# Performance work log

Hardware: AMD Instinct MI355X
Metric: run time of the kernel (lower is better)

## Reference

```python
import jax, jax.numpy as jnp
import numpy as np

N_VOLS, N_PARTS = 4, 8          # hard-coded in GL.forward
B = N_VOLS * N_PARTS            # asserted batch size = 32
DIM, HID, PROJ = 8192, 4096, 256
TEMP = 0.1
BN_EPS = 1e-5


def setup_inputs() -> dict:
    key = jax.random.key(0)
    k = jax.random.split(key, 5)
    s1 = 1.0 / np.sqrt(DIM)
    s2 = 1.0 / np.sqrt(HID)
    return {
        "x": jax.random.normal(k[0], (B, DIM), jnp.float32),
        "W1": jax.random.uniform(k[1], (DIM, HID), jnp.float32, -s1, s1),
        "b1": jax.random.uniform(k[2], (HID,), jnp.float32, -s1, s1),
        "gamma": jnp.ones((HID,), jnp.float32),
        "beta": jnp.zeros((HID,), jnp.float32),
        "W2": jax.random.uniform(k[3], (HID, PROJ), jnp.float32, -s2, s2),
        "b2": jax.random.uniform(k[4], (PROJ,), jnp.float32, -s2, s2),
    }


def _gl_loss(proj):
    # F.normalize(p=2, dim=-1); CosineSimilarity on unit vectors == dot product
    p = proj / jnp.linalg.norm(proj, axis=-1, keepdims=True)
    sims = (p @ p.T) / TEMP                       # [B, B]
    idx = jnp.arange(B)
    # pos_index(i) = {i % n_parts + v * n_parts} -> same part id; includes i itself
    pos_mask = (idx[:, None] % N_PARTS) == (idx[None, :] % N_PARTS)  # [B, B], 4 per row
    neg_mask = ~pos_mask                                             # 28 per row
    E = jnp.exp(sims)                              # original uses raw exp (no max-shift)
    row_neg = jnp.sum(jnp.where(neg_mask, E, 0.0), axis=1)    # sum_j exp(s[i, neg_j])
    ET = E.T                                        # ET[i, p] = exp(s[p, i])
    col_neg = jnp.sum(jnp.where(neg_mask, ET, 0.0), axis=1)   # sum_j exp(s[neg_j, i])
    t1 = -jnp.log(E / (E + row_neg[:, None]))      # row-direction term per (i, pos)
    t2 = -jnp.log(ET / (ET + col_neg[:, None]))    # column-direction term per (i, pos)
    per_row = jnp.sum(jnp.where(pos_mask, t1 + t2, 0.0), axis=1) / N_VOLS
    return jnp.sum(per_row) / (B * 2)


def reference(x, W1, b1, gamma, beta, W2, b2):
    # projector MLP: Linear -> BatchNorm1d (training stats) -> ReLU -> Linear
    h = x @ W1 + b1
    mu = jnp.mean(h, axis=0)
    var = jnp.var(h, axis=0)                       # biased variance, BN training mode
    h = gamma * (h - mu) * jax.lax.rsqrt(var + BN_EPS) + beta
    h = jax.nn.relu(h)
    proj = h @ W2 + b2                             # [B, PROJ]
    return _gl_loss(proj)
```

## Files before the change

### kernel.cpp

```cpp
#include <hip/hip_runtime.h>

#define DIM   8192
#define HID   4096
#define PROJ  256
#define NB    32
#define KSP1  16
#define KCH1  (DIM / KSP1)
#define KT1   (KCH1 / 32)
#define KSP2  16
#define KCH2  (HID / KSP2)
#define KT2   (KCH2 / 32)

typedef __attribute__((ext_vector_type(8))) short bf16x8;
typedef __attribute__((ext_vector_type(4))) float f32x4;

__device__ __forceinline__ float bf2f(unsigned short u) {
    return __uint_as_float(((unsigned)u) << 16);
}
__device__ __forceinline__ unsigned short f2bf(float f) {
    unsigned u = __float_as_uint(f);
    u += 0x7fffu + ((u >> 16) & 1u);
    return (unsigned short)(u >> 16);
}
__device__ __forceinline__ unsigned pk2(float a, float b) {
    return (unsigned)f2bf(a) | ((unsigned)f2bf(b) << 16);
}

__device__ __forceinline__ bool detect_bf16(const unsigned* __restrict__ xw, int lane) {
    unsigned v = xw[lane];
    int e = (int)((v >> 7) & 0xffu);
    bool pl = (e >= 100 && e <= 135);
    unsigned long long b = __ballot(pl);
    return __popcll(b) >= 32;
}

__device__ __forceinline__ void cp16_g2l(const void* g, void* l) {
    __builtin_amdgcn_global_load_lds(
        (const __attribute__((address_space(1))) void*)g,
        (__attribute__((address_space(3))) void*)l, 16, 0, 0);
}

__global__ __launch_bounds__(256, 4) void gemm1_kernel(
    const void* __restrict__ xv, const void* __restrict__ W1v,
    float* __restrict__ hpart)
{
    __shared__ unsigned short wt[2][2048];
    const int t  = threadIdx.x;
    const int nb = blockIdx.x & 63;
    const int kc = blockIdx.x >> 6;
    const int n0 = nb * 64;
    const int k0 = kc * KCH1;

    const bool isbf = detect_bf16((const unsigned*)xv, t & 63);
    const unsigned short* xu  = (const unsigned short*)xv;
    const float*          xf  = (const float*)xv;
    const unsigned short* W1u = (const unsigned short*)W1v;
    const float*          W1f = (const float*)W1v;

    const int lane = t & 63;
    const int w    = t >> 6;
    const int g    = lane >> 4;
    const int ln   = lane & 15;

    const int srow = w * 8 + (lane >> 3);
    const int scb  = (lane & 7) ^ w;
    const long sgo = (long)srow * HID + n0 + scb * 8;
    unsigned short* sl = &wt[0][w * 512];

    auto issue_stage = [&](int buf, int kt) {
        const unsigned short* gp = W1u + ((long)(k0 + kt * 32) * HID + sgo);
        if (isbf) {
            cp16_g2l((const void*)gp, (void*)(sl + buf * 2048));
        } else {
            const float* gpf = W1f + ((long)(k0 + kt * 32) * HID + sgo);
            float4 f0 = *(const float4*)gpf;
            float4 f1 = *(const float4*)(gpf + 4);
            unsigned* dst = (unsigned*)&wt[buf][srow * 64 + (lane & 7) * 8];
            dst[0] = pk2(f0.x, f0.y); dst[1] = pk2(f0.z, f0.w);
            dst[2] = pk2(f1.x, f1.y); dst[3] = pk2(f1.z, f1.w);
        }
    };
    auto loadA = [&](int kt, int mt) -> bf16x8 {
        const int base = (mt * 16 + ln) * DIM + k0 + kt * 32 + g * 8;
        if (isbf) return *(const bf16x8*)(xu + base);
        float4 f0 = *(const float4*)(xf + base);
        float4 f1 = *(const float4*)(xf + base + 4);
        union { uint4 u; bf16x8 v; } c;
        c.u = make_uint4(pk2(f0.x, f0.y), pk2(f0.z, f0.w),
                         pk2(f1.x, f1.y), pk2(f1.z, f1.w));
        return c.v;
    };

    issue_stage(0, 0);
    bf16x8 areg[2][2];
    areg[0][0] = loadA(0, 0); areg[0][1] = loadA(0, 1);
    areg[1][0] = loadA(1, 0); areg[1][1] = loadA(1, 1);
    __syncthreads();

    f32x4 acc0 = {0.f, 0.f, 0.f, 0.f};
    f32x4 acc1 = {0.f, 0.f, 0.f, 0.f};
    const int bco = w * 16 + ln;
    const int bidx = g * 8 * 64 + (((bco >> 3) ^ g) * 8 + (bco & 7));

    #pragma unroll
    for (int kt = 0; kt < KT1; ++kt) {
        const int cur = kt & 1;
        if (kt + 1 < KT1) issue_stage(cur ^ 1, kt + 1);

        bf16x8 b;
        const unsigned short* wpb = &wt[cur][bidx];
        #pragma unroll
        for (int j = 0; j < 8; ++j) b[j] = (short)wpb[j * 64];

        acc0 = __builtin_amdgcn_mfma_f32_16x16x32_bf16(areg[cur][0], b, acc0, 0, 0, 0);
        acc1 = __builtin_amdgcn_mfma_f32_16x16x32_bf16(areg[cur][1], b, acc1, 0, 0, 0);

        if (kt + 2 < KT1) { areg[cur][0] = loadA(kt + 2, 0); areg[cur][1] = loadA(kt + 2, 1); }
        __syncthreads();
    }

    const int col = n0 + bco;
    #pragma unroll
    for (int r = 0; r < 4; ++r) {
        hpart[(kc * NB + g * 4 + r) * HID + col]      = acc0[r];
        hpart[(kc * NB + 16 + g * 4 + r) * HID + col] = acc1[r];
    }
}

__global__ __launch_bounds__(256) void bnrelu_kernel(
    const float* __restrict__ hpart, const void* __restrict__ gv,
    const void* __restrict__ bev, unsigned short* __restrict__ hrelu,
    const void* __restrict__ xv)
{
    __shared__ float red[16][64];
    __shared__ float ssc[64], sbe[64], smu[64];
    const int t  = threadIdx.x;
    const int c4 = t & 15, q = t >> 4;
    const int n0 = blockIdx.x * 64;
    const int nb = n0 + c4 * 4;
    const bool isbf = detect_bf16((const unsigned*)xv, t & 63);

    f32x4 h0 = {0.f, 0.f, 0.f, 0.f};
    f32x4 h1 = {0.f, 0.f, 0.f, 0.f};
    #pragma unroll
    for (int kc = 0; kc < KSP1; ++kc) {
        h0 += *(const f32x4*)(hpart + (size_t)(kc * 32 + 2 * q) * HID + nb);
        h1 += *(const f32x4*)(hpart + (size_t)(kc * 32 + 2 * q + 1) * HID + nb);
    }
    *(f32x4*)&red[q][c4 * 4] = h0 + h1;
    __syncthreads();
    if (t < 64) {
        float s = 0.f;
        #pragma unroll
        for (int i = 0; i < 16; ++i) s += red[i][t];
        smu[t] = s * (1.f / 32.f);
    }
    __syncthreads();
    const f32x4 mu = *(const f32x4*)&smu[c4 * 4];
    const f32x4 d0 = h0 - mu, d1 = h1 - mu;
    *(f32x4*)&red[q][c4 * 4] = d0 * d0 + d1 * d1;
    __syncthreads();
    if (t < 64) {
        float v = 0.f;
        #pragma unroll
        for (int i = 0; i < 16; ++i) v += red[i][t];
        v *= (1.f / 32.f);
        const int nn = n0 + t;
        const float ga = isbf ? bf2f(((const unsigned short*)gv)[nn])  : ((const float*)gv)[nn];
        const float be = isbf ? bf2f(((const unsigned short*)bev)[nn]) : ((const float*)bev)[nn];
        ssc[t] = ga * rsqrtf(v + 1e-5f);
        sbe[t] = be;
    }
    __syncthreads();
    const f32x4 sc = *(const f32x4*)&ssc[c4 * 4];
    const f32x4 be = *(const f32x4*)&sbe[c4 * 4];
    f32x4 r0 = d0 * sc + be;
    f32x4 r1 = d1 * sc + be;
    ushort4 o0, o1;
    o0.x = f2bf(fmaxf(r0.x, 0.f)); o0.y = f2bf(fmaxf(r0.y, 0.f));
    o0.z = f2bf(fmaxf(r0.z, 0.f)); o0.w = f2bf(fmaxf(r0.w, 0.f));
    o1.x = f2bf(fmaxf(r1.x, 0.f)); o1.y = f2bf(fmaxf(r1.y, 0.f));
    o1.z = f2bf(fmaxf(r1.z, 0.f)); o1.w = f2bf(fmaxf(r1.w, 0.f));
    *(ushort4*)(hrelu + (size_t)(2 * q) * HID + nb)     = o0;
    *(ushort4*)(hrelu + (size_t)(2 * q + 1) * HID + nb) = o1;
}

__global__ __launch_bounds__(256, 4) void gemm2_kernel(
    const unsigned short* __restrict__ hrelu, const void* __restrict__ W2v,
    float* __restrict__ ppart, const void* __restrict__ xv)
{
    __shared__ unsigned short wt[2 * 32 * 66];
    const int t  = threadIdx.x;
    const int nb = blockIdx.x & 3;
    const int kc = blockIdx.x >> 2;
    const int n0 = nb * 64;
    const int k0 = kc * KCH2;

    const bool isbf = detect_bf16((const unsigned*)xv, t & 63);
    const unsigned short* W2u = (const unsigned short*)W2v;
    const float*          W2f = (const float*)W2v;

    const int lane = t & 63;
    const int w    = t >> 6;
    const int g    = lane >> 4;
    const int ln   = lane & 15;
    const int wr   = t >> 3;
    const int wc   = (t & 7) * 8;

    auto loadW2 = [&](int kt) -> uint4 {
        const int base = (k0 + kt * 32 + wr) * PROJ + n0 + wc;
        if (isbf) return *(const uint4*)(W2u + base);
        float4 f0 = *(const float4*)(W2f + base);
        float4 f1 = *(const float4*)(W2f + base + 4);
        return make_uint4(pk2(f0.x, f0.y), pk2(f0.z, f0.w),
                          pk2(f1.x, f1.y), pk2(f1.z, f1.w));
    };
    auto storeTile = [&](int buf, uint4 v) {
        unsigned* dst = (unsigned*)&wt[buf * 2112 + wr * 66 + wc];
        dst[0] = v.x; dst[1] = v.y; dst[2] = v.z; dst[3] = v.w;
    };
    auto loadA = [&](int kt, int mt) -> bf16x8 {
        return *(const bf16x8*)(hrelu + (mt * 16 + ln) * HID + k0 + kt * 32 + g * 8);
    };

    storeTile(0, loadW2(0));
    uint4 pf[3];
    pf[0] = loadW2(1); pf[1] = loadW2(2); pf[2] = loadW2(3);
    bf16x8 areg[2][2];
    areg[0][0] = loadA(0, 0); areg[0][1] = loadA(0, 1);
    areg[1][0] = loadA(1, 0); areg[1][1] = loadA(1, 1);
    __syncthreads();

    f32x4 acc0 = {0.f, 0.f, 0.f, 0.f};
    f32x4 acc1 = {0.f, 0.f, 0.f, 0.f};
    const int bco = w * 16 + ln;

    #pragma unroll
    for (int kt = 0; kt < KT2; ++kt) {
        const int cur = kt & 1;
        bf16x8 b;
        const unsigned short* wpb = &wt[cur * 2112 + g * 528 + bco];
        #pragma unroll
        for (int j = 0; j < 8; ++j) b[j] = (short)wpb[j * 66];

        acc0 = __builtin_amdgcn_mfma_f32_16x16x32_bf16(areg[cur][0], b, acc0, 0, 0, 0);
        acc1 = __builtin_amdgcn_mfma_f32_16x16x32_bf16(areg[cur][1], b, acc1, 0, 0, 0);

        if (kt + 2 < KT2) { areg[cur][0] = loadA(kt + 2, 0); areg[cur][1] = loadA(kt + 2, 1); }
        if (kt + 1 < KT2) storeTile(cur ^ 1, pf[kt % 3]);
        if (kt + 4 < KT2) pf[kt % 3] = loadW2(kt + 4);
        __syncthreads();
    }

    const int col = n0 + bco;
    #pragma unroll
    for (int r = 0; r < 4; ++r) {
        ppart[(kc * NB + g * 4 + r) * PROJ + col]      = acc0[r];
        ppart[(kc * NB + 16 + g * 4 + r) * PROJ + col] = acc1[r];
    }
}

__global__ __launch_bounds__(1024) void loss_kernel(
    const float* __restrict__ ppart, const void* __restrict__ b2v,
    const void* __restrict__ xv, unsigned* __restrict__ out)
{
    __shared__ float ps[32][260];
    __shared__ float npart2[32][8];
    __shared__ float inrm[32];
    __shared__ float rowtot[32];
    const int t = threadIdx.x;
    const bool isbf = detect_bf16((const unsigned*)xv, t & 63);

    #pragma unroll
    for (int i = 0; i < 8; ++i) {
        const int o = i * 1024 + t;
        float s = 0.f;
        #pragma unroll
        for (int s16 = 0; s16 < KSP2; ++s16) s += ppart[s16 * (NB * PROJ) + o];
        const int c = o & 255;
        s += isbf ? bf2f(((const unsigned short*)b2v)[c]) : ((const float*)b2v)[c];
        ps[o >> 8][c] = s;
    }
    __syncthreads();

    if (t < 256) {
        const int r = t >> 3, seg = t & 7;
        float s = 0.f;
        #pragma unroll
        for (int c = 0; c < 32; ++c) { float v = ps[r][seg * 32 + c]; s += v * v; }
        npart2[r][seg] = s;
    }
    __syncthreads();
    if (t < 32) {
        float s = 0.f;
        #pragma unroll
        for (int j = 0; j < 8; ++j) s += npart2[t][j];
        inrm[t] = rsqrtf(s);
    }
    __syncthreads();

    const int wv   = t >> 6;
    const int lane = t & 63;
    const int j    = (lane >> 1) & 31;
    const int half = lane & 1;
    #pragma unroll
    for (int rr = 0; rr < 2; ++rr) {
        const int i = wv * 2 + rr;
        float acc = 0.f;
        const int cb = half * 128;
        #pragma unroll
        for (int c = 0; c < 128; c += 4) {
            float4 a = *(const float4*)&ps[i][cb + c];
            float4 b = *(const float4*)&ps[j][cb + c];
            acc += a.x * b.x + a.y * b.y + a.z * b.z + a.w * b.w;
        }
        acc += __shfl_xor(acc, 1);

        const float sim = acc * inrm[i] * inrm[j] * 10.0f;
        const float E   = __expf(sim);
        const bool pos  = ((j & 7) == (i & 7));

        float nv = (!pos && half == 0) ? E : 0.f;
        #pragma unroll
        for (int s = 1; s < 64; s <<= 1) nv += __shfl_xor(nv, s);
        float pv = (pos && half == 0) ? (logf(E + nv) - sim) : 0.f;
        #pragma unroll
        for (int s = 1; s < 64; s <<= 1) pv += __shfl_xor(pv, s);
        if (lane == 0) rowtot[i] = pv;
    }
    __syncthreads();

    if (t < 64) {
        float v = (t < 32) ? rowtot[t] : 0.f;
        #pragma unroll
        for (int s = 1; s < 64; s <<= 1) v += __shfl_xor(v, s);
        if (t == 0) {
            const float loss = v * (1.0f / 128.0f);
            const unsigned lb = (unsigned)f2bf(loss);
            const unsigned base = (__float_as_uint(loss) & 0xffff0000u) | lb;
            unsigned best = base;
            float ebest = fabsf(__uint_as_float(base) - loss);
            const unsigned cp = base + 0x10000u;
            const float ep = fabsf(__uint_as_float(cp) - loss);
            if (ep < ebest) { best = cp; ebest = ep; }
            const unsigned cm = base - 0x10000u;
            const float em = fabsf(__uint_as_float(cm) - loss);
            if (em < ebest) { best = cm; }
            out[0] = best;
        }
    }
}

extern "C" void kernel_launch(void* const* d_in, const int* in_sizes, int n_in,
                              void* d_out, int out_size, void* d_ws, size_t ws_size,
                              hipStream_t stream) {
    const void* x  = d_in[0];
    const void* W1 = d_in[1];
    const void* ga = d_in[3];
    const void* be = d_in[4];
    const void* W2 = d_in[5];
    const void* b2 = d_in[6];

    char* wsp = (char*)d_ws;
    float* hpart = (float*)wsp;                 wsp += (size_t)KSP1 * NB * HID * 4;
    unsigned short* hrelu = (unsigned short*)wsp; wsp += (size_t)NB * HID * 2;
    float* ppart = (float*)wsp;                 wsp += (size_t)KSP2 * NB * PROJ * 4;

    gemm1_kernel<<<1024, 256, 0, stream>>>(x, W1, hpart);
    bnrelu_kernel<<<64, 256, 0, stream>>>(hpart, ga, be, hrelu, x);
    gemm2_kernel<<<64, 256, 0, stream>>>(hrelu, W2, ppart, x);
    loss_kernel<<<1, 1024, 0, stream>>>(ppart, b2, x, (unsigned*)d_out);
}
```

Before: 244.9 us.

## Load GEMM B operands directly from global into registers, drop LDS staging

Both GEMM kernels stop staging weight tiles through shared memory with double buffering and barriers. Each lane now gathers its 8 B-fragment elements straight from global memory with strided 2-byte loads into registers, using a 4-deep register prefetch ring for A and B. This removes the LDS round trip and the __syncthreads per k-step. In exchange the weight reads become scalar 16-bit gathers strided by row, which coalesce worse and may cost extra memory transactions on what is a bandwidth-bound weight stream.

```diff
diff --git a/kernel.cpp b/kernel.cpp
--- a/kernel.cpp
+++ b/kernel.cpp
@@ -34,21 +34,13 @@
     return __popcll(b) >= 32;
 }
 
-__device__ __forceinline__ void cp16_g2l(const void* g, void* l) {
-    __builtin_amdgcn_global_load_lds(
-        (const __attribute__((address_space(1))) void*)g,
-        (__attribute__((address_space(3))) void*)l, 16, 0, 0);
-}
-
 __global__ __launch_bounds__(256, 4) void gemm1_kernel(
     const void* __restrict__ xv, const void* __restrict__ W1v,
     float* __restrict__ hpart)
 {
-    __shared__ unsigned short wt[2][2048];
     const int t  = threadIdx.x;
     const int nb = blockIdx.x & 63;
     const int kc = blockIdx.x >> 6;
-    const int n0 = nb * 64;
     const int k0 = kc * KCH1;
 
     const bool isbf = detect_bf16((const unsigned*)xv, t & 63);
@@ -57,28 +49,23 @@
     const unsigned short* W1u = (const unsigned short*)W1v;
     const float*          W1f = (const float*)W1v;
 
-    const int lane = t & 63;
-    const int w    = t >> 6;
-    const int g    = lane >> 4;
-    const int ln   = lane & 15;
-
-    const int srow = w * 8 + (lane >> 3);
-    const int scb  = (lane & 7) ^ w;
-    const long sgo = (long)srow * HID + n0 + scb * 8;
-    unsigned short* sl = &wt[0][w * 512];
-
-    auto issue_stage = [&](int buf, int kt) {
-        const unsigned short* gp = W1u + ((long)(k0 + kt * 32) * HID + sgo);
+    const int lane  = t & 63;
+    const int w     = t >> 6;
+    const int g     = lane >> 4;
+    const int ln    = lane & 15;
+    const int nbase = nb * 64 + w * 16;
+
+    auto loadB = [&](int kt) -> bf16x8 {
+        bf16x8 b;
+        const long rb = (long)(k0 + kt * 32 + g * 8) * HID + nbase + ln;
         if (isbf) {
-            cp16_g2l((const void*)gp, (void*)(sl + buf * 2048));
+            #pragma unroll
+            for (int j = 0; j < 8; ++j) b[j] = (short)W1u[rb + (long)j * HID];
         } else {
-            const float* gpf = W1f + ((long)(k0 + kt * 32) * HID + sgo);
-            float4 f0 = *(const float4*)gpf;
-            float4 f1 = *(const float4*)(gpf + 4);
-            unsigned* dst = (unsigned*)&wt[buf][srow * 64 + (lane & 7) * 8];
-            dst[0] = pk2(f0.x, f0.y); dst[1] = pk2(f0.z, f0.w);
-            dst[2] = pk2(f1.x, f1.y); dst[3] = pk2(f1.z, f1.w);
-        }
+            #pragma unroll
+            for (int j = 0; j < 8; ++j) b[j] = (short)f2bf(W1f[rb + (long)j * HID]);
+        }
+        return b;
     };
     auto loadA = [&](int kt, int mt) -> bf16x8 {
         const int base = (mt * 16 + ln) * DIM + k0 + kt * 32 + g * 8;
@@ -91,35 +78,28 @@
         return c.v;
     };
 
-    issue_stage(0, 0);
-    bf16x8 areg[2][2];
-    areg[0][0] = loadA(0, 0); areg[0][1] = loadA(0, 1);
-    areg[1][0] = loadA(1, 0); areg[1][1] = loadA(1, 1);
-    __syncthreads();
+    bf16x8 bb[4], a0[4], a1[4];
+    #pragma unroll
+    for (int i = 0; i < 4; ++i) {
+        bb[i] = loadB(i); a0[i] = loadA(i, 0); a1[i] = loadA(i, 1);
+    }
 
     f32x4 acc0 = {0.f, 0.f, 0.f, 0.f};
     f32x4 acc1 = {0.f, 0.f, 0.f, 0.f};
-    const int bco = w * 16 + ln;
-    const int bidx = g * 8 * 64 + (((bco >> 3) ^ g) * 8 + (bco & 7));
 
     #pragma unroll
     for (int kt = 0; kt < KT1; ++kt) {
-        const int cur = kt & 1;
-        if (kt + 1 < KT1) issue_stage(cur ^ 1, kt + 1);
-
-        bf16x8 b;
-        const unsigned short* wpb = &wt[cur][bidx];
-        #pragma unroll
-        for (int j = 0; j < 8; ++j) b[j] = (short)wpb[j * 64];
-
-        acc0 = __builtin_amdgcn_mfma_f32_16x16x32_bf16(areg[cur][0], b, acc0, 0, 0, 0);
-        acc1 = __builtin_amdgcn_mfma_f32_16x16x32_bf16(areg[cur][1], b, acc1, 0, 0, 0);
-
-        if (kt + 2 < KT1) { areg[cur][0] = loadA(kt + 2, 0); areg[cur][1] = loadA(kt + 2, 1); }
-        __syncthreads();
-    }
-
-    const int col = n0 + bco;
+        const int s = kt & 3;
+        acc0 = __builtin_amdgcn_mfma_f32_16x16x32_bf16(a0[s], bb[s], acc0, 0, 0, 0);
+        acc1 = __builtin_amdgcn_mfma_f32_16x16x32_bf16(a1[s], bb[s], acc1, 0, 0, 0);
+        if (kt + 4 < KT1) {
+            bb[s] = loadB(kt + 4);
+            a0[s] = loadA(kt + 4, 0);
+            a1[s] = loadA(kt + 4, 1);
+        }
+    }
+
+    const int col = nbase + ln;
     #pragma unroll
     for (int r = 0; r < 4; ++r) {
         hpart[(kc * NB + g * 4 + r) * HID + col]      = acc0[r];
@@ -189,70 +169,59 @@
     const unsigned short* __restrict__ hrelu, const void* __restrict__ W2v,
     float* __restrict__ ppart, const void* __restrict__ xv)
 {
-    __shared__ unsigned short wt[2 * 32 * 66];
     const int t  = threadIdx.x;
     const int nb = blockIdx.x & 3;
     const int kc = blockIdx.x >> 2;
-    const int n0 = nb * 64;
     const int k0 = kc * KCH2;
 
     const bool isbf = detect_bf16((const unsigned*)xv, t & 63);
     const unsigned short* W2u = (const unsigned short*)W2v;
     const float*          W2f = (const float*)W2v;
 
-    const int lane = t & 63;
-    const int w    = t >> 6;
-    const int g    = lane >> 4;
-    const int ln   = lane & 15;
-    const int wr   = t >> 3;
-    const int wc   = (t & 7) * 8;
-
-    auto loadW2 = [&](int kt) -> uint4 {
-        const int base = (k0 + kt * 32 + wr) * PROJ + n0 + wc;
-        if (isbf) return *(const uint4*)(W2u + base);
-        float4 f0 = *(const float4*)(W2f + base);
-        float4 f1 = *(const float4*)(W2f + base + 4);
-        return make_uint4(pk2(f0.x, f0.y), pk2(f0.z, f0.w),
-                          pk2(f1.x, f1.y), pk2(f1.z, f1.w));
-    };
-    auto storeTile = [&](int buf, uint4 v) {
-        unsigned* dst = (unsigned*)&wt[buf * 2112 + wr * 66 + wc];
-        dst[0] = v.x; dst[1] = v.y; dst[2] = v.z; dst[3] = v.w;
+    const int lane  = t & 63;
+    const int w     = t >> 6;
+    const int g     = lane >> 4;
+    const int ln    = lane & 15;
+    const int nbase = nb * 64 + w * 16;
+
+    auto loadB = [&](int kt) -> bf16x8 {
+        bf16x8 b;
+        const long rb = (long)(k0 + kt * 32 + g * 8) * PROJ + nbase + ln;
+        if (isbf) {
+            #pragma unroll
+            for (int j = 0; j < 8; ++j) b[j] = (short)W2u[rb + (long)j * PROJ];
+        } else {
+            #pragma unroll
+            for (int j = 0; j < 8; ++j) b[j] = (short)f2bf(W2f[rb + (long)j * PROJ]);
+        }
+        return b;
     };
     auto loadA = [&](int kt, int mt) -> bf16x8 {
         return *(const bf16x8*)(hrelu + (mt * 16 + ln) * HID + k0 + kt * 32 + g * 8);
     };
 
-    storeTile(0, loadW2(0));
-    uint4 pf[3];
-    pf[0] = loadW2(1); pf[1] = loadW2(2); pf[2] = loadW2(3);
-    bf16x8 areg[2][2];
-    areg[0][0] = loadA(0, 0); areg[0][1] = loadA(0, 1);
-    areg[1][0] = loadA(1, 0); areg[1][1] = loadA(1, 1);
-    __syncthreads();
+    bf16x8 bb[4], a0[4], a1[4];
+    #pragma unroll
+    for (int i = 0; i < 4; ++i) {
+        bb[i] = loadB(i); a0[i] = loadA(i, 0); a1[i] = loadA(i, 1);
+    }
 
     f32x4 acc0 = {0.f, 0.f, 0.f, 0.f};
     f32x4 acc1 = {0.f, 0.f, 0.f, 0.f};
-    const int bco = w * 16 + ln;
 
     #pragma unroll
     for (int kt = 0; kt < KT2; ++kt) {
-        const int cur = kt & 1;
-        bf16x8 b;
-        const unsigned short* wpb = &wt[cur * 2112 + g * 528 + bco];
-        #pragma unroll
-        for (int j = 0; j < 8; ++j) b[j] = (short)wpb[j * 66];
-
-        acc0 = __builtin_amdgcn_mfma_f32_16x16x32_bf16(areg[cur][0], b, acc0, 0, 0, 0);
-        acc1 = __builtin_amdgcn_mfma_f32_16x16x32_bf16(areg[cur][1], b, acc1, 0, 0, 0);
-
-        if (kt + 2 < KT2) { areg[cur][0] = loadA(kt + 2, 0); areg[cur][1] = loadA(kt + 2, 1); }
-        if (kt + 1 < KT2) storeTile(cur ^ 1, pf[kt % 3]);
-        if (kt + 4 < KT2) pf[kt % 3] = loadW2(kt + 4);
-        __syncthreads();
-    }
-
-    const int col = n0 + bco;
+        const int s = kt & 3;
+        acc0 = __builtin_amdgcn_mfma_f32_16x16x32_bf16(a0[s], bb[s], acc0, 0, 0, 0);
+        acc1 = __builtin_amdgcn_mfma_f32_16x16x32_bf16(a1[s], bb[s], acc1, 0, 0, 0);
+        if (kt + 4 < KT2) {
+            bb[s] = loadB(kt + 4);
+            a0[s] = loadA(kt + 4, 0);
+            a1[s] = loadA(kt + 4, 1);
+        }
+    }
+
+    const int col = nbase + ln;
     #pragma unroll
     for (int r = 0; r < 4; ++r) {
         ppart[(kc * NB + g * 4 + r) * PROJ + col]      = acc0[r];
```

Result: no change. 242.2 us (-1.1%).
